# Optimization experiments

Measured on AMD Instinct MI355X. Metric: run time of the kernel, lower is better.

The kernel has to match this reference:

```python
import jax, jax.numpy as jnp
import numpy as np

N_NODES = 100000


def gcn_conv(x, W, b, src, dst, n):
    # PyG GCNConv: add self-loops, symmetric deg^-1/2 normalization,
    # transform then gather/scatter-add aggregate.
    loop = jnp.arange(n, dtype=src.dtype)
    s = jnp.concatenate([src, loop])
    d = jnp.concatenate([dst, loop])
    deg = jax.ops.segment_sum(jnp.ones_like(d, dtype=x.dtype), d, num_segments=n)
    dinv = jnp.where(deg > 0, 1.0 / jnp.sqrt(deg), 0.0)
    norm = dinv[s] * dinv[d]                      # [E+N]
    h = x @ W                                     # [N, out]
    msgs = h[s] * norm[:, None]                   # gather + scale
    out = jax.ops.segment_sum(msgs, d, num_segments=n)  # scatter-add
    return out + b


def setup_inputs() -> dict:
    key = jax.random.key(0)
    k1, k2, k3, k4 = jax.random.split(key, 4)
    F_in, H, D = 128, 16, 128
    x = jax.random.normal(k1, (N_NODES, F_in), dtype=jnp.float32)
    edge_index = jax.random.randint(k2, (2, 1600000), 0, N_NODES, dtype=jnp.int64)
    W1 = jax.random.normal(k3, (F_in, H), dtype=jnp.float32) / np.sqrt(F_in)
    b1 = jnp.zeros((H,), dtype=jnp.float32)
    W2 = jax.random.normal(k4, (H, D), dtype=jnp.float32) / np.sqrt(H)
    b2 = jnp.zeros((D,), dtype=jnp.float32)
    return {"x": x, "edge_index": edge_index, "W1": W1, "b1": b1, "W2": W2, "b2": b2}


def reference(x, edge_index, W1, b1, W2, b2):
    src, dst = edge_index[0], edge_index[1]
    n = x.shape[0]
    h = jax.nn.relu(gcn_conv(x, W1, b1, src, dst, n))
    out = jax.nn.relu(gcn_conv(h, W2, b2, src, dst, n))
    return out
```

## Files before the change

### kernel.cpp

```cpp
#include <hip/hip_runtime.h>
#include <hip/hip_fp16.h>
#include <stdint.h>

#define F_IN  128
#define HID   16
#define F_OUT 128
#define NBK   512
#define NBLK  512
#define BCAP  4096
#define CHUNK_MAX 4096
#define XP1   132
#define GT2_NODES 128

__device__ __forceinline__ int bucket_of(int d, int N) {
    return (int)(((long long)d * NBK) / N);
}
__device__ __forceinline__ int bucket_lo(int b, int N) {
    return (int)(((long long)b * N + NBK - 1) / NBK);
}

__global__ void __launch_bounds__(256) k_partf(
        const int* __restrict__ ei, int* __restrict__ bcur,
        uint32_t* __restrict__ pairs, int E, int N) {
    __shared__ int lh[NBK], lofs[NBK], lcur[NBK], gbase[NBK], lnlo[NBK];
    __shared__ int loff[256];
    __shared__ uint32_t spairs[CHUNK_MAX];
    __shared__ uint16_t sbkt[CHUNK_MAX];

    int blk = blockIdx.x, t = threadIdx.x;
    int Cr = (E + NBLK - 1) / NBLK;
    int C  = (Cr + 15) & ~15;
    int e0 = blk * C; if (e0 > E) e0 = E;
    int e1 = e0 + C;  if (e1 > E) e1 = E;
    int ecnt = e1 - e0;

    for (int i = t; i < NBK; i += 256) { lh[i] = 0; lnlo[i] = bucket_lo(i, N); }
    __syncthreads();

    int4 es4[4], ed4[4];
    bool evec = ((E & 3) == 0);
#pragma unroll
    for (int j = 0; j < 4; ++j) {
        int e = e0 + (j * 256 + t) * 4;
        if (evec && e + 4 <= e1) {
            es4[j] = *(const int4*)(ei + e);
            ed4[j] = *(const int4*)(ei + E + e);
        } else {
            int* s = (int*)&es4[j];
            int* d = (int*)&ed4[j];
#pragma unroll
            for (int q = 0; q < 4; ++q) {
                int ee = e + q;
                bool ok = (ee < e1);
                s[q] = ok ? ei[ee] : -1;
                d[q] = ok ? ei[E + ee] : 0;
            }
        }
    }
    const int* esv = (const int*)es4;
    const int* edv = (const int*)ed4;
    int eb[16];
#pragma unroll
    for (int k = 0; k < 16; ++k) {
        if (esv[k] >= 0) {
            eb[k] = bucket_of(edv[k], N);
            atomicAdd(&lh[eb[k]], 1);
        } else eb[k] = -1;
    }
    __syncthreads();

    int a0 = lh[2 * t], a1 = lh[2 * t + 1];
    int s2 = a0 + a1;
    loff[t] = s2;
    __syncthreads();
    for (int o = 1; o < 256; o <<= 1) {
        int a = (t >= o) ? loff[t - o] : 0;
        __syncthreads();
        loff[t] += a;
        __syncthreads();
    }
    int excl = loff[t] - s2;
    lofs[2 * t]     = excl;
    lofs[2 * t + 1] = excl + a0;
    lcur[2 * t]     = excl;
    lcur[2 * t + 1] = excl + a0;
    __syncthreads();

    for (int w = 0; w < NBK; w += 256) {
        int i = (t + w + blk) & (NBK - 1);
        int h = lh[i];
        gbase[i] = h ? atomicAdd(&bcur[i], h) : 0;
    }

#pragma unroll
    for (int k = 0; k < 16; ++k) {
        if (eb[k] >= 0) {
            int b = eb[k];
            int idx = atomicAdd(&lcur[b], 1);
            spairs[idx] = ((uint32_t)esv[k] << 10) | (uint32_t)(edv[k] - lnlo[b]);
            sbkt[idx]   = (uint16_t)b;
        }
    }
    __syncthreads();

    for (int i = t; i < ecnt; i += 256) {
        int b = sbkt[i];
        int pos = gbase[b] + (i - lofs[b]);
        if (pos < BCAP)
            pairs[(size_t)b * BCAP + pos] = spairs[i];
    }
}

__global__ void __launch_bounds__(256) k_csr2(
        const uint32_t* __restrict__ pairs, const int* __restrict__ bcur,
        int2* __restrict__ meta, float* __restrict__ dinv,
        int* __restrict__ srcs, int N) {
    __shared__ uint32_t sp[BCAP];
    __shared__ int lcnt[256];
    __shared__ int loff[256];
    __shared__ int lcur[256];
    int b = blockIdx.x, t = threadIdx.x;
    int base = b * BCAP;
    int ec = bcur[b]; if (ec > BCAP) ec = BCAP;
    int nlo = bucket_lo(b, N);
    int nhi = bucket_lo(b + 1, N); if (nhi > N) nhi = N;
    int nn = nhi - nlo;
    lcnt[t] = 0;
    __syncthreads();
    int ec4 = (ec + 3) >> 2;
    for (int i = t; i < ec4; i += 256) {
        uint4 v = *(const uint4*)(pairs + base + i * 4);
        *(uint4*)&sp[i * 4] = v;
        int lim = ec - i * 4;
        if (lim > 0) atomicAdd(&lcnt[v.x & 1023u], 1);
        if (lim > 1) atomicAdd(&lcnt[v.y & 1023u], 1);
        if (lim > 2) atomicAdd(&lcnt[v.z & 1023u], 1);
        if (lim > 3) atomicAdd(&lcnt[v.w & 1023u], 1);
    }
    __syncthreads();
    int v = lcnt[t];
    int pv = (v + 3) & ~3;
    loff[t] = pv;
    __syncthreads();
    for (int o = 1; o < 256; o <<= 1) {
        int a = (t >= o) ? loff[t - o] : 0;
        __syncthreads();
        loff[t] += a;
        __syncthreads();
    }
    if (t < nn) {
        int gs = base + (loff[t] - pv);
        meta[nlo + t] = make_int2(gs, v);
        dinv[nlo + t] = rsqrtf((float)(v + 1));
        lcur[t]       = gs;
    }
    __syncthreads();
    for (int e = t; e < ec; e += 256) {
        uint32_t p = sp[e];
        int pos = atomicAdd(&lcur[p & 1023u], 1);
        srcs[pos] = (int)(p >> 10);
    }
}

__global__ void __launch_bounds__(256) k_transform1(
        const float* __restrict__ x, const float* __restrict__ W1,
        const float* __restrict__ dinv, __half* __restrict__ g1, int n) {
    __shared__ float sX[32 * XP1];
    __shared__ float sWt[HID * XP1];
    int t = threadIdx.x;
    int node0 = blockIdx.x * 32;
    for (int i = t; i < F_IN * HID; i += 256) {
        int k = i >> 4, f = i & 15;
        sWt[f * XP1 + k] = W1[i];
    }
    const float4* x4 = (const float4*)(x + (size_t)node0 * F_IN);
    int nrem = n - node0;
#pragma unroll
    for (int j = 0; j < 4; ++j) {
        int idx4 = t + j * 256;
        int nl = idx4 >> 5;
        int kk = (idx4 & 31) * 4;
        float4 v = make_float4(0.f, 0.f, 0.f, 0.f);
        if (nl < nrem) v = x4[idx4];
        *(float4*)&sX[nl * XP1 + kk] = v;
    }
    __syncthreads();
    int f  = t & 7;
    int nl = t >> 3;
    float a0 = 0.f, a1 = 0.f;
    const float* xr  = &sX[nl * XP1];
    const float* wr0 = &sWt[f * XP1];
    const float* wr1 = &sWt[(f + 8) * XP1];
#pragma unroll 4
    for (int k = 0; k < F_IN; k += 4) {
        float4 xv = *(const float4*)(xr + k);
        float4 w0 = *(const float4*)(wr0 + k);
        float4 w1 = *(const float4*)(wr1 + k);
        a0 += xv.x * w0.x + xv.y * w0.y + xv.z * w0.z + xv.w * w0.w;
        a1 += xv.x * w1.x + xv.y * w1.y + xv.z * w1.z + xv.w * w1.w;
    }
    int node = node0 + nl;
    if (node < n) {
        float di = dinv[node];
        g1[(size_t)node * HID + f]     = __float2half(di * a0);
        g1[(size_t)node * HID + f + 8] = __float2half(di * a1);
    }
}

__device__ __forceinline__ void add_h8(float* __restrict__ acc, const __half* __restrict__ ptr) {
    uint4 u = *(const uint4*)ptr;
    const __half2* h = (const __half2*)&u;
#pragma unroll
    for (int q = 0; q < 4; ++q) {
        float2 f = __half22float2(h[q]);
        acc[2 * q]     += f.x;
        acc[2 * q + 1] += f.y;
    }
}

__device__ __forceinline__ void gather_acc(
        float* __restrict__ acc, int node, int p,
        const __half* __restrict__ g, const int* __restrict__ srcs,
        int rs, int deg) {
    {
        uint4 u = *(const uint4*)(g + (size_t)node * HID + p * 8);
        const __half2* h = (const __half2*)&u;
#pragma unroll
        for (int q = 0; q < 4; ++q) {
            float2 f = __half22float2(h[q]);
            acc[2 * q] = f.x; acc[2 * q + 1] = f.y;
        }
    }
    int j = 0;
    for (; j + 8 <= deg; j += 8) {
        int4 ia = *(const int4*)(srcs + rs + j);
        int4 ib = *(const int4*)(srcs + rs + j + 4);
        add_h8(acc, g + (size_t)ia.x * HID + p * 8);
        add_h8(acc, g + (size_t)ia.y * HID + p * 8);
        add_h8(acc, g + (size_t)ia.z * HID + p * 8);
        add_h8(acc, g + (size_t)ia.w * HID + p * 8);
        add_h8(acc, g + (size_t)ib.x * HID + p * 8);
        add_h8(acc, g + (size_t)ib.y * HID + p * 8);
        add_h8(acc, g + (size_t)ib.z * HID + p * 8);
        add_h8(acc, g + (size_t)ib.w * HID + p * 8);
    }
    if (j + 4 <= deg) {
        int4 ia = *(const int4*)(srcs + rs + j);
        add_h8(acc, g + (size_t)ia.x * HID + p * 8);
        add_h8(acc, g + (size_t)ia.y * HID + p * 8);
        add_h8(acc, g + (size_t)ia.z * HID + p * 8);
        add_h8(acc, g + (size_t)ia.w * HID + p * 8);
        j += 4;
    }
    for (; j < deg; ++j)
        add_h8(acc, g + (size_t)srcs[rs + j] * HID + p * 8);
}

__global__ void __launch_bounds__(256) k_gather1(
        const __half* __restrict__ g, const int* __restrict__ srcs,
        const int2* __restrict__ meta, const float* __restrict__ dinv,
        const float* __restrict__ b1, __half* __restrict__ outb, int n) {
    int tt = blockIdx.x * 256 + threadIdx.x;
    int node = tt >> 1;
    int p = tt & 1;
    if (node >= n) return;
    int2 m = meta[node];
    float acc[8];
    gather_acc(acc, node, p, g, srcs, m.x, m.y);
    float di = dinv[node];
#pragma unroll
    for (int i = 0; i < 8; ++i)
        acc[i] = di * fmaxf(di * acc[i] + b1[p * 8 + i], 0.0f);
    uint4 o;
    __half2* oh = (__half2*)&o;
#pragma unroll
    for (int q = 0; q < 4; ++q)
        oh[q] = __floats2half2_rn(acc[2 * q], acc[2 * q + 1]);
    *(uint4*)(outb + (size_t)node * HID + p * 8) = o;
}

__global__ void __launch_bounds__(256) k_gather_t2(
        const __half* __restrict__ g, const int* __restrict__ srcs,
        const int2* __restrict__ meta, const float* __restrict__ dinv,
        const float* __restrict__ W2, const float* __restrict__ b2,
        float* __restrict__ out, int n) {
    __shared__ __half sAgg[GT2_NODES * HID];
    __shared__ float  sdv[GT2_NODES];
    int t = threadIdx.x;
    int node0 = blockIdx.x * GT2_NODES;

    {
        int nl = t >> 1, p = t & 1;
        int node = node0 + nl;
        if (node < n) {
            if (p == 0) sdv[nl] = dinv[node];
            int2 m = meta[node];
            float acc[8];
            gather_acc(acc, node, p, g, srcs, m.x, m.y);
            uint4 o;
            __half2* oh = (__half2*)&o;
#pragma unroll
            for (int q = 0; q < 4; ++q)
                oh[q] = __floats2half2_rn(acc[2 * q], acc[2 * q + 1]);
            *(uint4*)&sAgg[nl * HID + p * 8] = o;
        }
    }
    __syncthreads();

    int d0 = (t & 31) * 4;
    int h  = t >> 5;
    float4 wcv[HID];
#pragma unroll
    for (int f2 = 0; f2 < HID; ++f2)
        wcv[f2] = *(const float4*)(W2 + f2 * F_OUT + d0);
    float4 bv = *(const float4*)(b2 + d0);
#pragma unroll 4
    for (int i = 0; i < GT2_NODES / 8; ++i) {
        int nl = h + 8 * i;
        int node = node0 + nl;
        if (node >= n) continue;
        const __half2* ah = (const __half2*)&sAgg[nl * HID];
        float4 s = make_float4(0.f, 0.f, 0.f, 0.f);
#pragma unroll
        for (int f2 = 0; f2 < HID; f2 += 2) {
            float2 fa = __half22float2(ah[f2 >> 1]);
            float4 w0 = wcv[f2], w1 = wcv[f2 + 1];
            s.x += fa.x * w0.x + fa.y * w1.x;
            s.y += fa.x * w0.y + fa.y * w1.y;
            s.z += fa.x * w0.z + fa.y * w1.z;
            s.w += fa.x * w0.w + fa.y * w1.w;
        }
        float dv = sdv[nl];
        float4 ov;
        ov.x = fmaxf(dv * s.x + bv.x, 0.f);
        ov.y = fmaxf(dv * s.y + bv.y, 0.f);
        ov.z = fmaxf(dv * s.z + bv.z, 0.f);
        ov.w = fmaxf(dv * s.w + bv.w, 0.f);
        *(float4*)(out + (size_t)node * F_OUT + d0) = ov;
    }
}

extern "C" void kernel_launch(void* const* d_in, const int* in_sizes, int n_in,
                              void* d_out, int out_size, void* d_ws, size_t ws_size,
                              hipStream_t stream) {
    const float* x  = (const float*)d_in[0];
    const int*   ei = (const int*)d_in[1];
    const float* W1 = (const float*)d_in[2];
    const float* b1 = (const float*)d_in[3];
    const float* W2 = (const float*)d_in[4];
    const float* b2 = (const float*)d_in[5];
    float* out = (float*)d_out;

    const int N = in_sizes[0] / F_IN;
    const int E = in_sizes[1] / 2;

    float* dinv      = (float*)d_ws;
    int2*  meta      = (int2*)(dinv + N);
    int*   bcur      = (int*)(meta + N);
    int*   srcs      = bcur + NBK;
    uint32_t* pairs  = (uint32_t*)(srcs + (size_t)NBK * BCAP);
    __half* bufA     = (__half*)(pairs + (size_t)NBK * BCAP);
    __half* bufB     = bufA + (size_t)N * HID;

    hipMemsetAsync(bcur, 0, NBK * sizeof(int), stream);
    k_partf<<<NBLK, 256, 0, stream>>>(ei, bcur, pairs, E, N);
    k_csr2 <<<NBK, 256, 0, stream>>>(pairs, bcur, meta, dinv, srcs, N);
    k_transform1<<<(N + 31) / 32, 256, 0, stream>>>(x, W1, dinv, bufA, N);
    k_gather1<<<((size_t)N * 2 + 255) / 256, 256, 0, stream>>>(
        bufA, srcs, meta, dinv, b1, bufB, N);
    k_gather_t2<<<(N + GT2_NODES - 1) / GT2_NODES, 256, 0, stream>>>(
        bufB, srcs, meta, dinv, W2, b2, out, N);
}
```

Before: 198.5 us.

## Use split-fp16 MFMA for both dense transforms

Replaces the scalar FP32 dot-product loops in the first-layer transform and the fused second-layer transform with MFMA matrix instructions. Operands are split into high and low fp16 parts, with three or two MFMAs per tile, to approximate fp32 accuracy. The first transform now handles 64 nodes per block. The second kernel writes output with scalar strided stores instead of float4, which may cost store efficiency.

```diff
diff --git a/kernel.cpp b/kernel.cpp
--- a/kernel.cpp
+++ b/kernel.cpp
@@ -9,8 +9,14 @@
 #define NBLK  512
 #define BCAP  4096
 #define CHUNK_MAX 4096
-#define XP1   132
 #define GT2_NODES 128
+#define T1N   64
+#define AGP   24
+
+typedef _Float16 f16;
+typedef f16 f16x4 __attribute__((ext_vector_type(4)));
+typedef f16 f16x8 __attribute__((ext_vector_type(8)));
+typedef float f32x4 __attribute__((ext_vector_type(4)));
 
 __device__ __forceinline__ int bucket_of(int d, int N) {
     return (int)(((long long)d * NBK) / N);
@@ -165,45 +171,62 @@
 __global__ void __launch_bounds__(256) k_transform1(
         const float* __restrict__ x, const float* __restrict__ W1,
         const float* __restrict__ dinv, __half* __restrict__ g1, int n) {
-    __shared__ float sX[32 * XP1];
-    __shared__ float sWt[HID * XP1];
+    __shared__ float sX[T1N * 132];
+    __shared__ float sW[128 * 17 + 4];
     int t = threadIdx.x;
-    int node0 = blockIdx.x * 32;
-    for (int i = t; i < F_IN * HID; i += 256) {
-        int k = i >> 4, f = i & 15;
-        sWt[f * XP1 + k] = W1[i];
-    }
-    const float4* x4 = (const float4*)(x + (size_t)node0 * F_IN);
-    int nrem = n - node0;
-#pragma unroll
-    for (int j = 0; j < 4; ++j) {
-        int idx4 = t + j * 256;
-        int nl = idx4 >> 5;
-        int kk = (idx4 & 31) * 4;
-        float4 v = make_float4(0.f, 0.f, 0.f, 0.f);
-        if (nl < nrem) v = x4[idx4];
-        *(float4*)&sX[nl * XP1 + kk] = v;
-    }
-    __syncthreads();
-    int f  = t & 7;
-    int nl = t >> 3;
-    float a0 = 0.f, a1 = 0.f;
-    const float* xr  = &sX[nl * XP1];
-    const float* wr0 = &sWt[f * XP1];
-    const float* wr1 = &sWt[(f + 8) * XP1];
-#pragma unroll 4
-    for (int k = 0; k < F_IN; k += 4) {
-        float4 xv = *(const float4*)(xr + k);
-        float4 w0 = *(const float4*)(wr0 + k);
-        float4 w1 = *(const float4*)(wr1 + k);
-        a0 += xv.x * w0.x + xv.y * w0.y + xv.z * w0.z + xv.w * w0.w;
-        a1 += xv.x * w1.x + xv.y * w1.y + xv.z * w1.z + xv.w * w1.w;
-    }
-    int node = node0 + nl;
-    if (node < n) {
-        float di = dinv[node];
-        g1[(size_t)node * HID + f]     = __float2half(di * a0);
-        g1[(size_t)node * HID + f + 8] = __float2half(di * a1);
+    int node0 = blockIdx.x * T1N;
+    for (int i = t; i < F_IN * HID; i += 256)
+        sW[(i >> 4) * 17 + (i & 15)] = W1[i];
+    {
+        const float4* xg = (const float4*)(x + (size_t)node0 * F_IN);
+        int nrem = n - node0;
+#pragma unroll
+        for (int j = 0; j < 8; ++j) {
+            int idx = t + j * 256;
+            int r = idx >> 5, c4 = idx & 31;
+            float4 v = make_float4(0.f, 0.f, 0.f, 0.f);
+            if (r < nrem) v = xg[idx];
+            *(float4*)&sX[r * 132 + c4 * 4] = v;
+        }
+    }
+    __syncthreads();
+    int lane = t & 63, wave = t >> 6;
+    int mcol = lane & 15, kg = lane >> 4;
+    f32x4 acc = {0.f, 0.f, 0.f, 0.f};
+#pragma unroll
+    for (int ks = 0; ks < 4; ++ks) {
+        int k0 = ks * 32 + kg * 8;
+        const float* xp = &sX[(wave * 16 + mcol) * 132 + k0];
+        float4 v0 = *(const float4*)xp;
+        float4 v1 = *(const float4*)(xp + 4);
+        float va[8] = {v0.x, v0.y, v0.z, v0.w, v1.x, v1.y, v1.z, v1.w};
+        f16x8 ah, al;
+#pragma unroll
+        for (int q = 0; q < 8; ++q) {
+            f16 h = (f16)va[q];
+            ah[q] = h;
+            al[q] = (f16)(va[q] - (float)h);
+        }
+        const float* wp = &sW[k0 * 17 + mcol];
+        f16x8 bh, bl;
+#pragma unroll
+        for (int q = 0; q < 8; ++q) {
+            float wv = wp[q * 17];
+            f16 h = (f16)wv;
+            bh[q] = h;
+            bl[q] = (f16)(wv - (float)h);
+        }
+        acc = __builtin_amdgcn_mfma_f32_16x16x32_f16(ah, bh, acc, 0, 0, 0);
+        acc = __builtin_amdgcn_mfma_f32_16x16x32_f16(al, bh, acc, 0, 0, 0);
+        acc = __builtin_amdgcn_mfma_f32_16x16x32_f16(ah, bl, acc, 0, 0, 0);
+    }
+#pragma unroll
+    for (int r = 0; r < 4; ++r) {
+        int node = node0 + wave * 16 + kg * 4 + r;
+        if (node < n) {
+            float di = dinv[node];
+            g1[(size_t)node * HID + mcol] = __float2half(di * acc[r]);
+        }
     }
 }
 
@@ -284,7 +307,7 @@
         const int2* __restrict__ meta, const float* __restrict__ dinv,
         const float* __restrict__ W2, const float* __restrict__ b2,
         float* __restrict__ out, int n) {
-    __shared__ __half sAgg[GT2_NODES * HID];
+    __shared__ __half sAgg[GT2_NODES * AGP];
     __shared__ float  sdv[GT2_NODES];
     int t = threadIdx.x;
     int node0 = blockIdx.x * GT2_NODES;
@@ -302,41 +325,58 @@
 #pragma unroll
             for (int q = 0; q < 4; ++q)
                 oh[q] = __floats2half2_rn(acc[2 * q], acc[2 * q + 1]);
-            *(uint4*)&sAgg[nl * HID + p * 8] = o;
-        }
-    }
-    __syncthreads();
-
-    int d0 = (t & 31) * 4;
-    int h  = t >> 5;
-    float4 wcv[HID];
-#pragma unroll
-    for (int f2 = 0; f2 < HID; ++f2)
-        wcv[f2] = *(const float4*)(W2 + f2 * F_OUT + d0);
-    float4 bv = *(const float4*)(b2 + d0);
-#pragma unroll 4
-    for (int i = 0; i < GT2_NODES / 8; ++i) {
-        int nl = h + 8 * i;
-        int node = node0 + nl;
-        if (node >= n) continue;
-        const __half2* ah = (const __half2*)&sAgg[nl * HID];
-        float4 s = make_float4(0.f, 0.f, 0.f, 0.f);
-#pragma unroll
-        for (int f2 = 0; f2 < HID; f2 += 2) {
-            float2 fa = __half22float2(ah[f2 >> 1]);
-            float4 w0 = wcv[f2], w1 = wcv[f2 + 1];
-            s.x += fa.x * w0.x + fa.y * w1.x;
-            s.y += fa.x * w0.y + fa.y * w1.y;
-            s.z += fa.x * w0.z + fa.y * w1.z;
-            s.w += fa.x * w0.w + fa.y * w1.w;
-        }
-        float dv = sdv[nl];
-        float4 ov;
-        ov.x = fmaxf(dv * s.x + bv.x, 0.f);
-        ov.y = fmaxf(dv * s.y + bv.y, 0.f);
-        ov.z = fmaxf(dv * s.z + bv.z, 0.f);
-        ov.w = fmaxf(dv * s.w + bv.w, 0.f);
-        *(float4*)(out + (size_t)node * F_OUT + d0) = ov;
+            *(uint4*)&sAgg[nl * AGP + p * 8] = o;
+        }
+    }
+    __syncthreads();
+
+    int lane = t & 63, wave = t >> 6;
+    int fcol = lane & 15, kg = lane >> 4;
+    int k0 = kg * 4;
+    f16x4 bh[8], bl[8];
+    float b2v[8];
+#pragma unroll
+    for (int nt = 0; nt < 8; ++nt) {
+        b2v[nt] = b2[nt * 16 + fcol];
+#pragma unroll
+        for (int j = 0; j < 4; ++j) {
+            float wv = W2[(k0 + j) * F_OUT + nt * 16 + fcol];
+            f16 h = (f16)wv;
+            bh[nt][j] = h;
+            bl[nt][j] = (f16)(wv - (float)h);
+        }
+    }
+    const f16* sA = (const f16*)sAgg;
+    f16x4 aA = *(const f16x4*)&sA[(wave * 32 + fcol) * AGP + k0];
+    f16x4 aB = *(const f16x4*)&sA[(wave * 32 + 16 + fcol) * AGP + k0];
+    f32x4 zero = {0.f, 0.f, 0.f, 0.f};
+    f32x4 acc[2][8];
+#pragma unroll
+    for (int mt = 0; mt < 2; ++mt)
+#pragma unroll
+        for (int nt = 0; nt < 8; ++nt)
+            acc[mt][nt] = zero;
+#pragma unroll
+    for (int nt = 0; nt < 8; ++nt) {
+        acc[0][nt] = __builtin_amdgcn_mfma_f32_16x16x16f16(aA, bh[nt], acc[0][nt], 0, 0, 0);
+        acc[0][nt] = __builtin_amdgcn_mfma_f32_16x16x16f16(aA, bl[nt], acc[0][nt], 0, 0, 0);
+        acc[1][nt] = __builtin_amdgcn_mfma_f32_16x16x16f16(aB, bh[nt], acc[1][nt], 0, 0, 0);
+        acc[1][nt] = __builtin_amdgcn_mfma_f32_16x16x16f16(aB, bl[nt], acc[1][nt], 0, 0, 0);
+    }
+#pragma unroll
+    for (int mt = 0; mt < 2; ++mt) {
+#pragma unroll
+        for (int r = 0; r < 4; ++r) {
+            int ln = wave * 32 + mt * 16 + kg * 4 + r;
+            int node = node0 + ln;
+            if (node < n) {
+                float dv = sdv[ln];
+#pragma unroll
+                for (int nt = 0; nt < 8; ++nt)
+                    out[(size_t)node * F_OUT + nt * 16 + fcol] =
+                        fmaxf(dv * acc[mt][nt][r] + b2v[nt], 0.f);
+            }
+        }
     }
 }
 
@@ -365,7 +405,7 @@
     hipMemsetAsync(bcur, 0, NBK * sizeof(int), stream);
     k_partf<<<NBLK, 256, 0, stream>>>(ei, bcur, pairs, E, N);
     k_csr2 <<<NBK, 256, 0, stream>>>(pairs, bcur, meta, dinv, srcs, N);
-    k_transform1<<<(N + 31) / 32, 256, 0, stream>>>(x, W1, dinv, bufA, N);
+    k_transform1<<<(N + T1N - 1) / T1N, 256, 0, stream>>>(x, W1, dinv, bufA, N);
     k_gather1<<<((size_t)N * 2 + 255) / 256, 256, 0, stream>>>(
         bufA, srcs, meta, dinv, b1, bufB, N);
     k_gather_t2<<<(N + GT2_NODES - 1) / GT2_NODES, 256, 0, stream>>>(
```

After: 196.9 us. No clear change (-0.8%).
